# Kernel optimization log

Hardware: AMD Instinct MI355X
Metric: run time of the kernel (lower is better)

Reference implementation:

```python
import jax, jax.numpy as jnp
from jax import lax
import numpy as np

COMMITMENT_COST = 0.25
N_EMBED = 512
EDIM = 32


def _conv(x, w, b, stride, pad):
    # x: NCHW, w: OIHW (torch Conv2d layout)
    y = lax.conv_general_dilated(x, w, (stride, stride), [(pad, pad), (pad, pad)],
                                 dimension_numbers=("NCHW", "OIHW", "NCHW"))
    return y + b[None, :, None, None]


def _conv_t(x, w, b, stride, pad):
    # torch ConvTranspose2d weight layout: (in, out, kH, kW)
    k = w.shape[2]
    w_ = jnp.flip(w, (2, 3)).transpose(1, 0, 2, 3)  # -> OIHW
    p = k - 1 - pad
    y = lax.conv_general_dilated(x, w_, (1, 1), [(p, p), (p, p)],
                                 lhs_dilation=(stride, stride),
                                 dimension_numbers=("NCHW", "OIHW", "NCHW"))
    return y + b[None, :, None, None]


def setup_inputs() -> dict:
    key = jax.random.key(0)
    ks = jax.random.split(key, 9)
    rn = lambda k, s: jax.random.normal(k, s, jnp.float32) * 0.05
    return {
        "x": jax.random.normal(ks[0], (32, 3, 256, 256), jnp.float32),
        "e_w1": rn(ks[1], (64, 3, 4, 4)),    "e_b1": jnp.zeros((64,), jnp.float32),
        "e_w2": rn(ks[2], (128, 64, 4, 4)),  "e_b2": jnp.zeros((128,), jnp.float32),
        "e_w3": rn(ks[3], (32, 128, 3, 3)),  "e_b3": jnp.zeros((32,), jnp.float32),
        "embed": jax.random.uniform(ks[4], (N_EMBED, EDIM), jnp.float32,
                                    -1.0 / N_EMBED, 1.0 / N_EMBED),
        "d_w1": rn(ks[5], (32, 128, 3, 3)),  "d_b1": jnp.zeros((128,), jnp.float32),
        "d_w2": rn(ks[6], (128, 64, 4, 4)),  "d_b2": jnp.zeros((64,), jnp.float32),
        "d_w3": rn(ks[7], (64, 3, 4, 4)),    "d_b3": jnp.zeros((3,), jnp.float32),
    }


def reference(x, e_w1, e_b1, e_w2, e_b2, e_w3, e_b3, embed,
              d_w1, d_b1, d_w2, d_b2, d_w3, d_b3):
    # ---- encoder ----
    h = jax.nn.relu(_conv(x, e_w1, e_b1, 2, 1))   # [B,64,128,128]
    h = jax.nn.relu(_conv(h, e_w2, e_b2, 2, 1))   # [B,128,64,64]
    z = jax.nn.relu(_conv(h, e_w3, e_b3, 1, 1))   # [B,32,64,64]
    # ---- vector quantizer ----
    zp = z.transpose(0, 2, 3, 1)                  # BHWC
    zf = zp.reshape(-1, EDIM)                     # [N, 32]
    d = (zf ** 2).sum(1, keepdims=True) + (embed ** 2).sum(1) \
        - 2.0 * zf @ embed.T                      # [N, n_embed]
    idx = jnp.argmin(d, axis=1)                   # [N]
    z_q = embed[idx].reshape(zp.shape)            # gather == onehot @ embed
    sg = lax.stop_gradient
    loss = jnp.mean((sg(z_q) - zp) ** 2) + COMMITMENT_COST * jnp.mean((z_q - sg(zp)) ** 2)
    z_q_st = zp + sg(z_q - zp)                    # straight-through
    z_q_st = z_q_st.transpose(0, 3, 1, 2)         # back to NCHW
    # ---- decoder ----
    h = jax.nn.relu(_conv_t(z_q_st, d_w1, d_b1, 1, 1))  # [B,128,64,64]
    h = jax.nn.relu(_conv_t(h, d_w2, d_b2, 2, 1))       # [B,64,128,128]
    x_recon = _conv_t(h, d_w3, d_b3, 2, 1)              # [B,3,256,256]
    return x_recon, loss
```

## Files before the change

### kernel.cpp

```cpp
#include <hip/hip_runtime.h>


typedef __attribute__((ext_vector_type(8))) short     short8;
typedef __attribute__((ext_vector_type(4))) short     s16x4;
typedef __attribute__((ext_vector_type(8))) __bf16    bf16x8;
typedef __attribute__((ext_vector_type(4))) float     f32x4;
typedef __attribute__((ext_vector_type(4))) unsigned  uint32x4;

__device__ __forceinline__ float b2f(unsigned short b) {
  union { unsigned u; float f; } v; v.u = ((unsigned)b) << 16; return v.f;
}
__device__ __forceinline__ unsigned short f2b(float f) {
  union { float f; unsigned u; } v; v.f = f;
  unsigned r = v.u + 0x7FFF + ((v.u >> 16) & 1);
  return (unsigned short)(r >> 16);
}

__global__ __launch_bounds__(256) void prep1v_k(const float* __restrict__ w,
                                                unsigned short* __restrict__ wq) {
  const int i = blockIdx.x*256 + threadIdx.x;
  const int j = i & 7, l = (i >> 3) & 63, ni = (i >> 9) & 3, ks = i >> 11;
  const int k = ks*32 + (l >> 4)*8 + j;
  const int co = ni*16 + (l & 15);
  wq[i] = (k < 48) ? f2b(w[co*48 + k]) : (unsigned short)0;
}
__global__ __launch_bounds__(256) void prep2v_k(const float* __restrict__ w,
                                                unsigned short* __restrict__ wq) {
  const int i = blockIdx.x*256 + threadIdx.x;
  const int j = i & 7, l = (i >> 3) & 63, ni = (i >> 9) & 7, ks = i >> 12;
  const int lm = l & 15, lk = l >> 4;
  const int tap = ks >> 1, cc = ks & 1;
  const int co = ni*16 + lm, ci = cc*32 + lk*8 + j;
  wq[i] = f2b(w[(co*64 + ci)*16 + tap]);
}
__global__ __launch_bounds__(256) void prep3v_k(const float* __restrict__ w,
                                                unsigned short* __restrict__ wq) {
  const int i = blockIdx.x*256 + threadIdx.x;
  const int j = i & 7, l = (i >> 3) & 63, ni = (i >> 9) & 1, ks = i >> 10;
  const int lm = l & 15, lk = l >> 4;
  const int tap = ks >> 2, cf = ks & 3;
  const int co = ni*16 + lm, ci = cf*32 + lk*8 + j;
  wq[i] = f2b(w[(co*128 + ci)*9 + tap]);
}
__global__ __launch_bounds__(256) void prep4v_k(const float* __restrict__ w,
                                                unsigned short* __restrict__ wq) {
  const int i = blockIdx.x*256 + threadIdx.x;
  const int j = i & 7, l = (i >> 3) & 63, ni = (i >> 9) & 7, tap = i >> 12;
  const int lm = l & 15, lk = l >> 4;
  const int co = ni*16 + lm, ci = lk*8 + j;
  wq[i] = f2b(w[(ci*128 + co)*9 + (8 - tap)]);
}
__global__ __launch_bounds__(256) void prep5v_k(const float* __restrict__ w,
                                                unsigned short* __restrict__ wq) {
  const int i = blockIdx.x*256 + threadIdx.x;
  const int j = i & 7, l = (i >> 3) & 63, ni = (i >> 9) & 3;
  const int ks = (i >> 11) & 15, p = i >> 15;
  const int lm = l & 15, lk = l >> 4;
  const int py = p >> 1, px = p & 1;
  const int a = ks >> 3, b = (ks >> 2) & 1, cc = ks & 3;
  const int co = ni*16 + lm, ci = cc*32 + lk*8 + j;
  const int ky = 3 - 2*a - py, kx = 3 - 2*b - px;
  wq[i] = f2b(w[(ci*64 + co)*16 + ky*4 + kx]);
}
__global__ __launch_bounds__(256) void prep6_k(const float* __restrict__ w,
                                               unsigned short* __restrict__ wq) {
  const int i = blockIdx.x*256 + threadIdx.x;
  const int j = i & 7, l = (i >> 3) & 63, kc = (i >> 9) & 7, p = i >> 12;
  const int lm = l & 15, lk = l >> 4;
  const int a = kc >> 2, b = (kc >> 1) & 1, ch = kc & 1;
  const int ci = ch*32 + lk*8 + j, co = lm;
  const int py = p >> 1, px = p & 1;
  const int ky = 2 - 2*a + (1 - py), kx = 2 - 2*b + (1 - px);
  wq[i] = (co < 3) ? f2b(w[(ci*3 + co)*16 + ky*4 + kx]) : (unsigned short)0;
}
__global__ __launch_bounds__(256) void prepe_k(const float* __restrict__ emb,
    unsigned short* __restrict__ wqe, float* __restrict__ en) {
  const int i = blockIdx.x*256 + threadIdx.x;
  const int j = i & 7, l = (i >> 3) & 63, ni = (i >> 9) & 3, nc = i >> 11;
  const int lm = l & 15, lk = l >> 4;
  wqe[i] = f2b(emb[(nc*64 + ni*16 + lm)*32 + lk*8 + j]);
  if (i < 512) {
    float s = 0.f;
    #pragma unroll
    for (int k = 0; k < 32; ++k) {
      const float f = b2f(f2b(emb[i*32 + k]));
      s = fmaf(f, f, s);
    }
    en[i] = s;
  }
}

__global__ __launch_bounds__(256) void conv1m_k(const float* __restrict__ x,
    const unsigned short* __restrict__ wv, const float* __restrict__ bias,
    unsigned short* __restrict__ out) {
  __shared__ __align__(16) short RAW[12*264];
  __shared__ __align__(16) short IC[128*64];
  const int wid = ((blockIdx.x & 7) << 9) + (blockIdx.x >> 3);
  const int q = wid & 127, n = wid >> 7;
  for (int i = threadIdx.x; i < 396; i += 256)
    *(short8*)&RAW[i*8] = (short8)(short)0;
  __syncthreads();
  for (int s = threadIdx.x; s < 768; s += 256) {
    const int g = s >> 6, seg = s & 63;
    const int ci = g >> 2, ky = g & 3;
    const int iy = 2*q - 1 + ky;
    if (iy >= 0 && iy < 256) {
      const f32x4 v = *(const f32x4*)&x[((n*3 + ci)*256 + iy)*256 + seg*4];
      s16x4 sv;
      #pragma unroll
      for (int e = 0; e < 4; ++e) sv[e] = (short)f2b(v[e]);
      *(s16x4*)&RAW[g*264 + 4 + seg*4] = sv;
    }
  }
  __syncthreads();
  for (int s = threadIdx.x; s < 1024; s += 256) {
    const int kb = s & 7, ox = s >> 3;
    short8 v = (short8)(short)0;
    if (kb < 6) {
      const unsigned* u0 = (const unsigned*)&RAW[(2*kb  )*264 + 2*ox + 2];
      const unsigned* u1 = (const unsigned*)&RAW[(2*kb+1)*264 + 2*ox + 2];
      const unsigned a0 = u0[0], a1 = u0[1], a2 = u0[2];
      const unsigned b0 = u1[0], b1 = u1[1], b2 = u1[2];
      uint32x4 uv;
      uv[0] = (a0 >> 16) | (a1 << 16);
      uv[1] = (a1 >> 16) | (a2 << 16);
      uv[2] = (b0 >> 16) | (b1 << 16);
      uv[3] = (b1 >> 16) | (b2 << 16);
      v = __builtin_bit_cast(short8, uv);
    }
    const int bo = ((ox << 7) + (kb << 4)) ^ ((ox & 7) << 4);
    *(short8*)((char*)IC + bo) = v;
  }
  __syncthreads();
  const int w = threadIdx.x >> 6, l = threadIdx.x & 63;
  const int lm = l & 15, lk = l >> 4;
  f32x4 acc[2][4];
  #pragma unroll
  for (int mi = 0; mi < 2; ++mi)
    #pragma unroll
    for (int ni = 0; ni < 4; ++ni) acc[mi][ni] = (f32x4)0.0f;
  #pragma unroll
  for (int ks = 0; ks < 2; ++ks) {
    short8 bv[4];
    #pragma unroll
    for (int ni = 0; ni < 4; ++ni)
      bv[ni] = *(const short8*)(wv + (((ks*4 + ni)*64 + l) << 3));
    #pragma unroll
    for (int mi = 0; mi < 2; ++mi) {
      const int ox = w*32 + mi*16 + lm;
      const int bo = ((ox << 7) + (ks << 6) + (lk << 4)) ^ ((ox & 7) << 4);
      const short8 av = *(const short8*)((const char*)IC + bo);
      #pragma unroll
      for (int ni = 0; ni < 4; ++ni)
        acc[mi][ni] = __builtin_amdgcn_mfma_f32_16x16x32_bf16(
            __builtin_bit_cast(bf16x8, av),
            __builtin_bit_cast(bf16x8, bv[ni]),
            acc[mi][ni], 0, 0, 0);
    }
  }
  __syncthreads();
  #pragma unroll
  for (int mi = 0; mi < 2; ++mi)
    #pragma unroll
    for (int ni = 0; ni < 4; ++ni) {
      const int co = ni*16 + lm;
      const float bv = bias[co];
      #pragma unroll
      for (int r = 0; r < 4; ++r) {
        const int ox = w*32 + mi*16 + lk*4 + r;
        const int bo = ((ox << 7) + 2*co) ^ ((ox & 7) << 4);
        *(short*)((char*)IC + bo) = (short)f2b(fmaxf(acc[mi][ni][r] + bv, 0.f));
      }
    }
  __syncthreads();
  const long ob = ((long)(n*128 + q)) * 8192;
  for (int s = threadIdx.x; s < 1024; s += 256) {
    const int kb = s & 7, ox = s >> 3;
    const int bo = ((ox << 7) + (kb << 4)) ^ ((ox & 7) << 4);
    *(short8*)&out[ob + ox*64 + kb*8] = *(const short8*)((const char*)IC + bo);
  }
}

#define C2_LOAD(c) \
  _Pragma("unroll") \
  for (int s = 0; s < 9; ++s) { \
    st[s] = (short8)(short)0; \
    if (goff[s] >= 0) st[s] = *(const short8*)(in + goff[s] + (c)*32); \
  }
#define C2_WRITE \
  _Pragma("unroll") \
  for (int s = 0; s < 9; ++s) \
    if (lb[s] >= 0) *(short8*)((char*)IL + lb[s]) = st[s];
#define C2_COMPUTE(c) \
  _Pragma("unroll") \
  for (int t = 0; t < 16; ++t) { \
    const int ky = t >> 2, kx = t & 3; \
    const int p = 1 - (kx & 1), d = kx >> 1; \
    const short8 bv0 = *(const short8*)(wb + (t*2 + (c))*4096); \
    const short8 bv1 = *(const short8*)(wb + (t*2 + (c))*4096 + 512); \
    const char* Ab = (const char*)IL + (Bd0 + d*64); \
    const int imm0 = ((ky*2 + p)*66) << 6; \
    _Pragma("unroll") \
    for (int mi = 0; mi < 4; ++mi) { \
      const short8 av = *(const short8*)(Ab + imm0 + mi*1024); \
      acc[mi][0] = __builtin_amdgcn_mfma_f32_16x16x32_bf16( \
          __builtin_bit_cast(bf16x8, av), __builtin_bit_cast(bf16x8, bv0), \
          acc[mi][0], 0, 0, 0); \
      acc[mi][1] = __builtin_amdgcn_mfma_f32_16x16x32_bf16( \
          __builtin_bit_cast(bf16x8, av), __builtin_bit_cast(bf16x8, bv1), \
          acc[mi][1], 0, 0, 0); \
    } \
  }
__global__ __launch_bounds__(256) void conv2m_k(const unsigned short* __restrict__ in,
    const unsigned short* __restrict__ wv, const float* __restrict__ bias,
    unsigned short* __restrict__ out) {
  __shared__ short IL[8*66*32];
  const int wid = (blockIdx.x & 7)*256 + (blockIdx.x >> 3);
  const int q = wid & 63, n = wid >> 6;
  const int w = threadIdx.x >> 6, l = threadIdx.x & 63;
  const int lm = l & 15, lk = l >> 4;
  const int Bd0 = lm*64 + lk*16;
  const unsigned short* wb = wv + w*1024 + l*8;
  int goff[9], lb[9];
  #pragma unroll
  for (int s = 0; s < 9; ++s) {
    const int i = threadIdx.x + s*256;
    const int part = i & 3, e = i >> 2;
    const int idx = e % 66, rp = e / 66;
    const int r = rp >> 1, p = rp & 1;
    const int iy = 2*q - 1 + r, ix = 2*idx - p;
    const bool ok = (i < 2112) && iy >= 0 && iy < 128 && ix >= 0 && ix < 128;
    goff[s] = ok ? (((n*128 + iy)*128 + ix)*64 + part*8) : -1;
    lb[s]   = (i < 2112) ? (e*64 + part*16) : -1;
  }
  f32x4 acc[4][2];
  #pragma unroll
  for (int mi = 0; mi < 4; ++mi)
    #pragma unroll
    for (int ni = 0; ni < 2; ++ni) acc[mi][ni] = (f32x4)0.0f;
  short8 st[9];
  C2_LOAD(0); C2_WRITE;
  __syncthreads();
  C2_LOAD(1);
  C2_COMPUTE(0);
  __syncthreads();
  C2_WRITE;
  __syncthreads();
  C2_COMPUTE(1);
  #pragma unroll
  for (int mi = 0; mi < 4; ++mi)
    #pragma unroll
    for (int r = 0; r < 4; ++r) {
      const int ox = mi*16 + lk*4 + r;
      const int ob = ((n*64 + q)*64 + ox)*128;
      #pragma unroll
      for (int ni = 0; ni < 2; ++ni) {
        const int co = (w*2 + ni)*16 + lm;
        out[ob + co] = f2b(fmaxf(acc[mi][ni][r] + bias[co], 0.f));
      }
    }
}

#define C3_LOAD(c) \
  _Pragma("unroll") \
  for (int s = 0; s < 9; ++s) { \
    st[s] = (short8)(short)0; \
    if (goff[s] >= 0) st[s] = *(const short8*)(in + goff[s] + (c)*64); \
  }
#define C3_WRITE \
  _Pragma("unroll") \
  for (int s = 0; s < 9; ++s) \
    if (lb[s] >= 0) *(short8*)((char*)IL + lb[s]) = st[s];
#define C3_COMPUTE(c) \
  _Pragma("unroll") \
  for (int u = 0; u < 18; ++u) { \
    const int tap = u >> 1, cc = u & 1; \
    const int ky = tap / 3, kx = tap % 3; \
    const int ks = tap*4 + (c)*2 + cc; \
    const short8 bv0 = *(const short8*)(wb + ks*1024); \
    const short8 bv1 = *(const short8*)(wb + ks*1024 + 512); \
    const char* Ab = (const char*)IL + (Wc[kx][cc]); \
    const int imm0 = ky*8448; \
    _Pragma("unroll") \
    for (int mi = 0; mi < 2; ++mi) { \
      const short8 av = *(const short8*)(Ab + imm0 + mi*2048); \
      acc[mi][0] = __builtin_amdgcn_mfma_f32_16x16x32_bf16( \
          __builtin_bit_cast(bf16x8, av), __builtin_bit_cast(bf16x8, bv0), \
          acc[mi][0], 0, 0, 0); \
      acc[mi][1] = __builtin_amdgcn_mfma_f32_16x16x32_bf16( \
          __builtin_bit_cast(bf16x8, av), __builtin_bit_cast(bf16x8, bv1), \
          acc[mi][1], 0, 0, 0); \
    } \
  }
__global__ __launch_bounds__(256) void conv3v_k(const unsigned short* __restrict__ in,
    const unsigned short* __restrict__ wv, const float* __restrict__ bias,
    const unsigned short* __restrict__ wqe, const float* __restrict__ eng,
    const float* __restrict__ emb, float* __restrict__ zq,
    float* __restrict__ part) {
  __shared__ short IL[4*66*64];
  const int wid = (blockIdx.x & 7)*128 + (blockIdx.x >> 3);
  const int q = wid & 31, n = wid >> 5;
  const int w = threadIdx.x >> 6, l = threadIdx.x & 63;
  const int lm = l & 15, lk = l >> 4;
  const int row = w >> 1, oxb = (w & 1) * 32;
  int goff[9], lb[9];
  #pragma unroll
  for (int s = 0; s < 9; ++s) {
    const int i = threadIdx.x + s*256;
    const int part_ = i & 7, e = i >> 3;
    const int col = e % 66, r = e / 66;
    const int iy = 2*q - 1 + r, ix = col - 1;
    const bool ok = (i < 2112) && iy >= 0 && iy < 64 && ix >= 0 && ix < 64;
    goff[s] = ok ? (((n*64 + iy)*64 + ix)*128 + part_*8) : -1;
    lb[s]   = (i < 2112) ? ((e << 7) + ((part_ << 4) ^ ((col & 7) << 4))) : -1;
  }
  int Wc[3][2];
  #pragma unroll
  for (int kx = 0; kx < 3; ++kx) {
    const int e = oxb + lm + kx;
    Wc[kx][0] = row*8448 + (e << 7) + ((lk << 4) ^ ((e & 7) << 4));
    Wc[kx][1] = Wc[kx][0] ^ 0x40;
  }
  const unsigned short* wb = wv + l*8;
  f32x4 acc[2][2];
  #pragma unroll
  for (int mi = 0; mi < 2; ++mi)
    #pragma unroll
    for (int ni = 0; ni < 2; ++ni) acc[mi][ni] = (f32x4)0.0f;
  short8 st[9];
  C3_LOAD(0); C3_WRITE;
  __syncthreads();
  C3_LOAD(1);
  C3_COMPUTE(0);
  __syncthreads();
  C3_WRITE;
  __syncthreads();
  C3_COMPUTE(1);
  __syncthreads();
  short* ZB  = (short*)IL;
  float* ZF  = (float*)((char*)IL + 10240);
  int*  bidx = (int*)((char*)IL + 28672);
  float* red = (float*)((char*)IL + 29184);
  #pragma unroll
  for (int mi = 0; mi < 2; ++mi)
    #pragma unroll
    for (int ni = 0; ni < 2; ++ni) {
      const int co = ni*16 + lm;
      const float bv = bias[co];
      #pragma unroll
      for (int r = 0; r < 4; ++r) {
        const int pos = row*64 + oxb + mi*16 + lk*4 + r;
        const float v = fmaxf(acc[mi][ni][r] + bv, 0.f);
        ZB[pos*40 + co] = (short)f2b(v);
        ZF[pos*36 + co] = v;
      }
    }
  __syncthreads();
  short8 av[2];
  #pragma unroll
  for (int mi = 0; mi < 2; ++mi)
    av[mi] = *(const short8*)&ZB[(row*64 + oxb + mi*16 + lm)*40 + lk*8];
  float bd[2][4]; int bj[2][4];
  #pragma unroll
  for (int mi = 0; mi < 2; ++mi)
    #pragma unroll
    for (int r = 0; r < 4; ++r) { bd[mi][r] = 1e30f; bj[mi][r] = 0; }
  for (int nc = 0; nc < 8; ++nc) {
    f32x4 a2[2][4];
    #pragma unroll
    for (int mi = 0; mi < 2; ++mi)
      #pragma unroll
      for (int ni = 0; ni < 4; ++ni) a2[mi][ni] = (f32x4)0.0f;
    #pragma unroll
    for (int ni = 0; ni < 4; ++ni) {
      const short8 bv = *(const short8*)(wqe + (((nc*4 + ni)*64 + l) << 3));
      #pragma unroll
      for (int mi = 0; mi < 2; ++mi)
        a2[mi][ni] = __builtin_amdgcn_mfma_f32_16x16x32_bf16(
            __builtin_bit_cast(bf16x8, av[mi]),
            __builtin_bit_cast(bf16x8, bv),
            a2[mi][ni], 0, 0, 0);
    }
    #pragma unroll
    for (int ni = 0; ni < 4; ++ni) {
      const int j = nc*64 + ni*16 + lm;
      const float e_n = eng[j];
      #pragma unroll
      for (int mi = 0; mi < 2; ++mi)
        #pragma unroll
        for (int r = 0; r < 4; ++r) {
          const float d = fmaf(-2.f, a2[mi][ni][r], e_n);
          if (d < bd[mi][r]) { bd[mi][r] = d; bj[mi][r] = j; }
        }
    }
  }
  #pragma unroll
  for (int mi = 0; mi < 2; ++mi)
    #pragma unroll
    for (int r = 0; r < 4; ++r) {
      float d = bd[mi][r]; int j = bj[mi][r];
      #pragma unroll
      for (int off = 1; off < 16; off <<= 1) {
        const float od = __shfl_xor(d, off);
        const int   oj = __shfl_xor(j, off);
        if (od < d || (od == d && oj < j)) { d = od; j = oj; }
      }
      if (lm == 0) bidx[row*64 + oxb + mi*16 + lk*4 + r] = j;
    }
  __syncthreads();
  const int pl = threadIdx.x >> 1, hf = (threadIdx.x & 1) * 16;
  const int code = bidx[pl];
  const int oy2 = 2*q + (pl >> 6), ox2 = pl & 63;
  const long zqo = ((long)((n*64 + oy2)*64 + ox2)) * 32 + hf;
  float se = 0.f;
  #pragma unroll
  for (int qq = 0; qq < 4; ++qq) {
    const f32x4 ev = *(const f32x4*)&emb[code*32 + hf + qq*4];
    const f32x4 zv = *(const f32x4*)&ZF[pl*36 + hf + qq*4];
    *(f32x4*)&zq[zqo + qq*4] = ev;
    const f32x4 df = ev - zv;
    #pragma unroll
    for (int e = 0; e < 4; ++e) se = fmaf(df[e], df[e], se);
  }
  red[threadIdx.x] = se; __syncthreads();
  for (int s2 = 128; s2 > 0; s2 >>= 1) {
    if (threadIdx.x < s2) red[threadIdx.x] += red[threadIdx.x + s2];
    __syncthreads();
  }
  if (threadIdx.x == 0) part[blockIdx.x] = red[0];
}

__global__ __launch_bounds__(256) void d1m_k(const float* __restrict__ in,
    const unsigned short* __restrict__ wv, const float* __restrict__ bias,
    unsigned short* __restrict__ out) {
  __shared__ short IL[264*40];
  const int wid = (blockIdx.x & 7)*128 + (blockIdx.x >> 3);
  const int q = wid & 31, n = wid >> 5;
  const int w = threadIdx.x >> 6, l = threadIdx.x & 63;
  const int lm = l & 15, lk = l >> 4;
  const int row = w >> 1, oxb = (w & 1) * 32;
  for (int i = threadIdx.x; i < 1056; i += 256) {
    const int part = i & 3, e = i >> 2;
    const int col = e % 66, r = e / 66;
    const int iy = 2*q - 1 + r, ix = col - 1;
    short8 v = (short8)(short)0;
    if (iy >= 0 && iy < 64 && ix >= 0 && ix < 64) {
      const float* p = in + (((long)((n*64 + iy)*64 + ix)) * 32 + part*8);
      const f32x4 f0 = *(const f32x4*)p;
      const f32x4 f1 = *(const f32x4*)(p + 4);
      #pragma unroll
      for (int e2 = 0; e2 < 4; ++e2) {
        v[e2]     = (short)f2b(f0[e2]);
        v[e2 + 4] = (short)f2b(f1[e2]);
      }
    }
    *(short8*)&IL[e*40 + part*8] = v;
  }
  const unsigned short* wb = wv + l*8;
  int Wd[3];
  #pragma unroll
  for (int kx = 0; kx < 3; ++kx)
    Wd[kx] = row*5280 + (oxb + lm + kx)*80 + lk*16;
  __syncthreads();
  f32x4 acc[2][8];
  #pragma unroll
  for (int mi = 0; mi < 2; ++mi)
    #pragma unroll
    for (int ni = 0; ni < 8; ++ni) acc[mi][ni] = (f32x4)0.0f;
  #pragma unroll
  for (int tap = 0; tap < 9; ++tap) {
    const int ky = tap / 3, kx = tap % 3;
    short8 bv[8];
    #pragma unroll
    for (int ni = 0; ni < 8; ++ni)
      bv[ni] = *(const short8*)(wb + (tap*8 + ni)*512);
    const char* Ab = (const char*)IL + Wd[kx];
    const int imm0 = ky*5280;
    #pragma unroll
    for (int mi = 0; mi < 2; ++mi) {
      const short8 av = *(const short8*)(Ab + imm0 + mi*1280);
      #pragma unroll
      for (int ni = 0; ni < 8; ++ni)
        acc[mi][ni] = __builtin_amdgcn_mfma_f32_16x16x32_bf16(
            __builtin_bit_cast(bf16x8, av),
            __builtin_bit_cast(bf16x8, bv[ni]),
            acc[mi][ni], 0, 0, 0);
    }
  }
  const int oy = 2*q + row;
  #pragma unroll
  for (int mi = 0; mi < 2; ++mi)
    #pragma unroll
    for (int r = 0; r < 4; ++r) {
      const int ox = oxb + mi*16 + lk*4 + r;
      const int ob = ((n*64 + oy)*64 + ox)*128;
      #pragma unroll
      for (int ni = 0; ni < 8; ++ni) {
        const int co = ni*16 + lm;
        out[ob + co] = f2b(fmaxf(acc[mi][ni][r] + bias[co], 0.f));
      }
    }
}

#define CT2_LOAD(c) \
  _Pragma("unroll") \
  for (int s = 0; s < 7; ++s) { \
    st[s] = (short8)(short)0; \
    if (goff[s] >= 0) st[s] = *(const short8*)(in + goff[s] + (c)*64); \
  }
#define CT2_WRITE \
  _Pragma("unroll") \
  for (int s = 0; s < 7; ++s) \
    if (lb[s] >= 0) *(short8*)((char*)IL + lb[s]) = st[s];
#define CT2_COMPUTE(c) \
  _Pragma("unroll") \
  for (int u = 0; u < 8; ++u) { \
    const int a = u >> 2, b = (u >> 1) & 1, c1 = u & 1; \
    const int ks = (a << 3) | (b << 2) | (2*(c) + c1); \
    short8 bv[4]; \
    _Pragma("unroll") \
    for (int ni = 0; ni < 4; ++ni) \
      bv[ni] = *(const short8*)(wb + ks*2048 + ni*512); \
    const char* Ab = (const char*)IL + (pyb + Wb[b][c1]); \
    const int imm0 = a*8448; \
    _Pragma("unroll") \
    for (int mi = 0; mi < 4; ++mi) { \
      const short8 av = *(const short8*)(Ab + imm0 + mi*2048); \
      _Pragma("unroll") \
      for (int ni = 0; ni < 4; ++ni) \
        acc[mi][ni] = __builtin_amdgcn_mfma_f32_16x16x32_bf16( \
            __builtin_bit_cast(bf16x8, av), \
            __builtin_bit_cast(bf16x8, bv[ni]), \
            acc[mi][ni], 0, 0, 0); \
    } \
  }
__global__ __launch_bounds__(256) void convt2m_k(const unsigned short* __restrict__ in,
    const unsigned short* __restrict__ wv, const float* __restrict__ bias,
    unsigned short* __restrict__ out) {
  __shared__ short IL[3*66*64];
  const int wid = (blockIdx.x & 7)*256 + (blockIdx.x >> 3);
  const int q = wid & 63, n = wid >> 6;
  const int w = threadIdx.x >> 6, l = threadIdx.x & 63;
  const int py = w >> 1, px = w & 1;
  const int lm = l & 15, lk = l >> 4;
  int Wb[2][2];
  #pragma unroll
  for (int b = 0; b < 2; ++b) {
    const int e = lm + px + b;
    Wb[b][0] = (e << 7) + ((lk << 4) ^ ((e & 7) << 4));
    Wb[b][1] = Wb[b][0] ^ 0x40;
  }
  const int pyb = py * 8448;
  const unsigned short* wb = wv + w*32768 + l*8;
  int goff[7], lb[7];
  #pragma unroll
  for (int s = 0; s < 7; ++s) {
    const int i = threadIdx.x + s*256;
    const int part = i & 7, e = i >> 3;
    const int col = e % 66, r = e / 66;
    const int iy = q - 1 + r, ix = col - 1;
    const bool ok = (i < 1584) && iy >= 0 && iy < 64 && ix >= 0 && ix < 64;
    goff[s] = ok ? (((n*64 + iy)*64 + ix)*128 + part*8) : -1;
    lb[s]   = (i < 1584) ? ((e << 7) + ((part << 4) ^ ((col & 7) << 4))) : -1;
  }
  f32x4 acc[4][4];
  #pragma unroll
  for (int mi = 0; mi < 4; ++mi)
    #pragma unroll
    for (int ni = 0; ni < 4; ++ni) acc[mi][ni] = (f32x4)0.0f;
  short8 st[7];
  CT2_LOAD(0); CT2_WRITE;
  __syncthreads();
  CT2_LOAD(1);
  CT2_COMPUTE(0);
  __syncthreads();
  CT2_WRITE;
  __syncthreads();
  CT2_COMPUTE(1);
  const int oy = 2*q + py;
  #pragma unroll
  for (int mi = 0; mi < 4; ++mi)
    #pragma unroll
    for (int r = 0; r < 4; ++r) {
      const int ox = 2*(mi*16 + lk*4 + r) + px;
      const int ob = ((n*128 + oy)*128 + ox)*64;
      #pragma unroll
      for (int ni = 0; ni < 4; ++ni) {
        const int co = ni*16 + lm;
        out[ob + co] = f2b(fmaxf(acc[mi][ni][r] + bias[co], 0.f));
      }
    }
}

__global__ __launch_bounds__(256) void loss_k(const float* __restrict__ part,
                                              float* __restrict__ out) {
  __shared__ float red[256];
  const int t = threadIdx.x;
  float s = 0.f;
  #pragma unroll
  for (int q = 0; q < 4; ++q) s += part[t + q*256];
  red[t] = s; __syncthreads();
  for (int st = 128; st > 0; st >>= 1) {
    if (t < st) red[t] += red[t + st];
    __syncthreads();
  }
  if (t == 0) out[0] = red[0] * (1.25f / (131072.f * 32.f));
}

__global__ __launch_bounds__(256) void convt3m_k(const unsigned short* __restrict__ in,
    const unsigned short* __restrict__ wq6, const float* __restrict__ bias,
    float* __restrict__ out) {
  __shared__ short8 IL[3*8*66];
  const int h = blockIdx.x & 1, q = (blockIdx.x >> 1) & 127, n = blockIdx.x >> 8;
  for (int i = threadIdx.x; i < 1584; i += 256) {
    const int c8 = i & 7, t = i >> 3, ixl = t % 66, r = t / 66;
    const int iy = q - 1 + r, ix = h*64 - 1 + ixl;
    short8 v = (short8)(short)0;
    if (iy >= 0 && iy < 128 && ix >= 0 && ix < 128)
      v = *(const short8*)(in + (((long)(n*128 + iy)*128 + ix)*64 + c8*8));
    IL[(r*8 + c8)*66 + ixl] = v;
  }
  const int w = threadIdx.x >> 6, l = threadIdx.x & 63;
  const int py = w >> 1, px = w & 1;
  const int lm = l & 15, lk = l >> 4;
  short8 bfrag[8];
  #pragma unroll
  for (int kc = 0; kc < 8; ++kc)
    bfrag[kc] = *(const short8*)(wq6 + (((w*8 + kc)*64 + l) << 3));
  __syncthreads();
  f32x4 acc[4];
  #pragma unroll
  for (int mi = 0; mi < 4; ++mi) acc[mi] = (f32x4)0.0f;
  #pragma unroll
  for (int kc = 0; kc < 8; ++kc) {
    const int a = kc >> 2, b = (kc >> 1) & 1, ch = kc & 1;
    const int base = (((py + a)*8 + ch*4 + lk)*66) + px + b;
    #pragma unroll
    for (int mi = 0; mi < 4; ++mi) {
      const short8 av = *(const short8*)&IL[base + mi*16 + lm];
      acc[mi] = __builtin_amdgcn_mfma_f32_16x16x32_bf16(
          __builtin_bit_cast(bf16x8, av),
          __builtin_bit_cast(bf16x8, bfrag[kc]),
          acc[mi], 0, 0, 0);
    }
  }
  if (lm < 3) {
    const float bv = bias[lm];
    const int oy = 2*q + py;
    const long ob = ((long)(n*3 + lm))*65536 + oy*256;
    #pragma unroll
    for (int mi = 0; mi < 4; ++mi)
      #pragma unroll
      for (int r = 0; r < 4; ++r) {
        const int xq = mi*16 + lk*4 + r;
        out[ob + h*128 + 2*xq + px] = acc[mi][r] + bv;
      }
  }
}

extern "C" void kernel_launch(void* const* d_in, const int* in_sizes, int n_in,
                              void* d_out, int out_size, void* d_ws, size_t ws_size,
                              hipStream_t stream) {
  const float* x   = (const float*)d_in[0];
  const float* ew1 = (const float*)d_in[1];  const float* eb1 = (const float*)d_in[2];
  const float* ew2 = (const float*)d_in[3];  const float* eb2 = (const float*)d_in[4];
  const float* ew3 = (const float*)d_in[5];  const float* eb3 = (const float*)d_in[6];
  const float* emb = (const float*)d_in[7];
  const float* dw1 = (const float*)d_in[8];  const float* db1 = (const float*)d_in[9];
  const float* dw2 = (const float*)d_in[10]; const float* db2 = (const float*)d_in[11];
  const float* dw3 = (const float*)d_in[12]; const float* db3 = (const float*)d_in[13];
  float* out = (float*)d_out;

  uint8_t* w8 = (uint8_t*)d_ws;
  unsigned short* h1 = (unsigned short*)w8;
  unsigned short* h2 = (unsigned short*)(w8 + 67108864);
  uint8_t* zr = w8 + 100663296;
  float* zq  = (float*)(w8 + 117440512);
  unsigned short* wqe = (unsigned short*)zr;
  float* eng = (float*)(zr + 32768);
  float* part = (float*)(zr + 36864);
  unsigned short* wq3 = (unsigned short*)(zr + 40960);
  unsigned short* wq4 = (unsigned short*)(zr + 131072);
  unsigned short* wq5 = (unsigned short*)(zr + 262144);
  unsigned short* wq6 = (unsigned short*)(zr + 524288);
  unsigned short* wq2 = (unsigned short*)(w8 + 117440512);
  unsigned short* wq1 = (unsigned short*)(w8 + 117440512 + 335872);
  unsigned short* d1 = h2;
  unsigned short* d2 = h1;

  prepe_k<<<dim3(64),256,0,stream>>>(emb, wqe, eng);
  prep1v_k<<<dim3(16),256,0,stream>>>(ew1, wq1);
  prep2v_k<<<dim3(512),256,0,stream>>>(ew2, wq2);
  prep3v_k<<<dim3(144),256,0,stream>>>(ew3, wq3);
  prep4v_k<<<dim3(144),256,0,stream>>>(dw1, wq4);
  prep5v_k<<<dim3(512),256,0,stream>>>(dw2, wq5);
  prep6_k<<<dim3(64),256,0,stream>>>(dw3, wq6);
  conv1m_k<<<dim3(4096),256,0,stream>>>(x, wq1, eb1, h1);
  conv2m_k<<<dim3(2048),256,0,stream>>>(h1, wq2, eb2, h2);
  conv3v_k<<<dim3(1024),256,0,stream>>>(h2, wq3, eb3, wqe, eng, emb, zq, part);
  loss_k<<<dim3(1),256,0,stream>>>(part, out + 6291456);
  d1m_k<<<dim3(1024),256,0,stream>>>(zq, wq4, db1, d1);
  convt2m_k<<<dim3(2048),256,0,stream>>>(d1, wq5, db2, d2);
  convt3m_k<<<dim3(8192),256,0,stream>>>(d2, wq6, db3, out);
}
```

Before: 355.8 us.

## Stage conv epilogues through LDS for coalesced stores; merge weight prep kernels

Four conv kernels (conv2, decoder conv1, convt2, convt3) now write their bias+ReLU results into shared memory first. They then emit contiguous 16-byte vector stores (or coalesced row stores for the final fp32 output) instead of scattered 2-byte per-lane global writes. The seven weight-preparation kernels are merged into one launch with block-range dispatch to cut launch overhead. The staging adds extra barriers and reuses the input LDS buffer, which must be large enough for the padded tiles.

```diff
diff --git a/kernel.cpp b/kernel.cpp
--- a/kernel.cpp
+++ b/kernel.cpp
@@ -16,77 +16,75 @@
   return (unsigned short)(r >> 16);
 }
 
-__global__ __launch_bounds__(256) void prep1v_k(const float* __restrict__ w,
-                                                unsigned short* __restrict__ wq) {
-  const int i = blockIdx.x*256 + threadIdx.x;
-  const int j = i & 7, l = (i >> 3) & 63, ni = (i >> 9) & 3, ks = i >> 11;
-  const int k = ks*32 + (l >> 4)*8 + j;
-  const int co = ni*16 + (l & 15);
-  wq[i] = (k < 48) ? f2b(w[co*48 + k]) : (unsigned short)0;
-}
-__global__ __launch_bounds__(256) void prep2v_k(const float* __restrict__ w,
-                                                unsigned short* __restrict__ wq) {
-  const int i = blockIdx.x*256 + threadIdx.x;
-  const int j = i & 7, l = (i >> 3) & 63, ni = (i >> 9) & 7, ks = i >> 12;
-  const int lm = l & 15, lk = l >> 4;
-  const int tap = ks >> 1, cc = ks & 1;
-  const int co = ni*16 + lm, ci = cc*32 + lk*8 + j;
-  wq[i] = f2b(w[(co*64 + ci)*16 + tap]);
-}
-__global__ __launch_bounds__(256) void prep3v_k(const float* __restrict__ w,
-                                                unsigned short* __restrict__ wq) {
-  const int i = blockIdx.x*256 + threadIdx.x;
-  const int j = i & 7, l = (i >> 3) & 63, ni = (i >> 9) & 1, ks = i >> 10;
-  const int lm = l & 15, lk = l >> 4;
-  const int tap = ks >> 2, cf = ks & 3;
-  const int co = ni*16 + lm, ci = cf*32 + lk*8 + j;
-  wq[i] = f2b(w[(co*128 + ci)*9 + tap]);
-}
-__global__ __launch_bounds__(256) void prep4v_k(const float* __restrict__ w,
-                                                unsigned short* __restrict__ wq) {
-  const int i = blockIdx.x*256 + threadIdx.x;
-  const int j = i & 7, l = (i >> 3) & 63, ni = (i >> 9) & 7, tap = i >> 12;
-  const int lm = l & 15, lk = l >> 4;
-  const int co = ni*16 + lm, ci = lk*8 + j;
-  wq[i] = f2b(w[(ci*128 + co)*9 + (8 - tap)]);
-}
-__global__ __launch_bounds__(256) void prep5v_k(const float* __restrict__ w,
-                                                unsigned short* __restrict__ wq) {
-  const int i = blockIdx.x*256 + threadIdx.x;
-  const int j = i & 7, l = (i >> 3) & 63, ni = (i >> 9) & 3;
-  const int ks = (i >> 11) & 15, p = i >> 15;
-  const int lm = l & 15, lk = l >> 4;
-  const int py = p >> 1, px = p & 1;
-  const int a = ks >> 3, b = (ks >> 2) & 1, cc = ks & 3;
-  const int co = ni*16 + lm, ci = cc*32 + lk*8 + j;
-  const int ky = 3 - 2*a - py, kx = 3 - 2*b - px;
-  wq[i] = f2b(w[(ci*64 + co)*16 + ky*4 + kx]);
-}
-__global__ __launch_bounds__(256) void prep6_k(const float* __restrict__ w,
-                                               unsigned short* __restrict__ wq) {
-  const int i = blockIdx.x*256 + threadIdx.x;
-  const int j = i & 7, l = (i >> 3) & 63, kc = (i >> 9) & 7, p = i >> 12;
-  const int lm = l & 15, lk = l >> 4;
-  const int a = kc >> 2, b = (kc >> 1) & 1, ch = kc & 1;
-  const int ci = ch*32 + lk*8 + j, co = lm;
-  const int py = p >> 1, px = p & 1;
-  const int ky = 2 - 2*a + (1 - py), kx = 2 - 2*b + (1 - px);
-  wq[i] = (co < 3) ? f2b(w[(ci*3 + co)*16 + ky*4 + kx]) : (unsigned short)0;
-}
-__global__ __launch_bounds__(256) void prepe_k(const float* __restrict__ emb,
-    unsigned short* __restrict__ wqe, float* __restrict__ en) {
-  const int i = blockIdx.x*256 + threadIdx.x;
-  const int j = i & 7, l = (i >> 3) & 63, ni = (i >> 9) & 3, nc = i >> 11;
-  const int lm = l & 15, lk = l >> 4;
-  wqe[i] = f2b(emb[(nc*64 + ni*16 + lm)*32 + lk*8 + j]);
-  if (i < 512) {
-    float s = 0.f;
-    #pragma unroll
-    for (int k = 0; k < 32; ++k) {
-      const float f = b2f(f2b(emb[i*32 + k]));
-      s = fmaf(f, f, s);
-    }
-    en[i] = s;
+__global__ __launch_bounds__(256) void prepall_k(
+    const float* __restrict__ ew1, const float* __restrict__ ew2,
+    const float* __restrict__ ew3, const float* __restrict__ dw1,
+    const float* __restrict__ dw2, const float* __restrict__ dw3,
+    const float* __restrict__ emb,
+    unsigned short* __restrict__ wq1, unsigned short* __restrict__ wq2,
+    unsigned short* __restrict__ wq3, unsigned short* __restrict__ wq4,
+    unsigned short* __restrict__ wq5, unsigned short* __restrict__ wq6,
+    unsigned short* __restrict__ wqe, float* __restrict__ eng) {
+  const int b = blockIdx.x;
+  if (b < 64) {
+    const int i = b*256 + threadIdx.x;
+    const int j = i & 7, l = (i >> 3) & 63, ni = (i >> 9) & 3, nc = i >> 11;
+    const int lm = l & 15, lk = l >> 4;
+    wqe[i] = f2b(emb[(nc*64 + ni*16 + lm)*32 + lk*8 + j]);
+    if (i < 512) {
+      float s = 0.f;
+      #pragma unroll
+      for (int k = 0; k < 32; ++k) {
+        const float f = b2f(f2b(emb[i*32 + k]));
+        s = fmaf(f, f, s);
+      }
+      eng[i] = s;
+    }
+  } else if (b < 80) {
+    const int i = (b - 64)*256 + threadIdx.x;
+    const int j = i & 7, l = (i >> 3) & 63, ni = (i >> 9) & 3, ks = i >> 11;
+    const int k = ks*32 + (l >> 4)*8 + j;
+    const int co = ni*16 + (l & 15);
+    wq1[i] = (k < 48) ? f2b(ew1[co*48 + k]) : (unsigned short)0;
+  } else if (b < 592) {
+    const int i = (b - 80)*256 + threadIdx.x;
+    const int j = i & 7, l = (i >> 3) & 63, ni = (i >> 9) & 7, ks = i >> 12;
+    const int lm = l & 15, lk = l >> 4;
+    const int tap = ks >> 1, cc = ks & 1;
+    const int co = ni*16 + lm, ci = cc*32 + lk*8 + j;
+    wq2[i] = f2b(ew2[(co*64 + ci)*16 + tap]);
+  } else if (b < 736) {
+    const int i = (b - 592)*256 + threadIdx.x;
+    const int j = i & 7, l = (i >> 3) & 63, ni = (i >> 9) & 1, ks = i >> 10;
+    const int lm = l & 15, lk = l >> 4;
+    const int tap = ks >> 2, cf = ks & 3;
+    const int co = ni*16 + lm, ci = cf*32 + lk*8 + j;
+    wq3[i] = f2b(ew3[(co*128 + ci)*9 + tap]);
+  } else if (b < 880) {
+    const int i = (b - 736)*256 + threadIdx.x;
+    const int j = i & 7, l = (i >> 3) & 63, ni = (i >> 9) & 7, tap = i >> 12;
+    const int lm = l & 15, lk = l >> 4;
+    const int co = ni*16 + lm, ci = lk*8 + j;
+    wq4[i] = f2b(dw1[(ci*128 + co)*9 + (8 - tap)]);
+  } else if (b < 1392) {
+    const int i = (b - 880)*256 + threadIdx.x;
+    const int j = i & 7, l = (i >> 3) & 63, ni = (i >> 9) & 3;
+    const int ks = (i >> 11) & 15, p = i >> 15;
+    const int lm = l & 15, lk = l >> 4;
+    const int py = p >> 1, px = p & 1;
+    const int a = ks >> 3, bb = (ks >> 2) & 1, cc = ks & 3;
+    const int co = ni*16 + lm, ci = cc*32 + lk*8 + j;
+    const int ky = 3 - 2*a - py, kx = 3 - 2*bb - px;
+    wq5[i] = f2b(dw2[(ci*64 + co)*16 + ky*4 + kx]);
+  } else {
+    const int i = (b - 1392)*256 + threadIdx.x;
+    const int j = i & 7, l = (i >> 3) & 63, kc = (i >> 9) & 7, p = i >> 12;
+    const int lm = l & 15, lk = l >> 4;
+    const int a = kc >> 2, bb = (kc >> 1) & 1, ch = kc & 1;
+    const int ci = ch*32 + lk*8 + j, co = lm;
+    const int py = p >> 1, px = p & 1;
+    const int ky = 2 - 2*a + (1 - py), kx = 2 - 2*bb + (1 - px);
+    wq6[i] = (co < 3) ? f2b(dw3[(ci*3 + co)*16 + ky*4 + kx]) : (unsigned short)0;
   }
 }
 
@@ -247,18 +245,27 @@
   C2_WRITE;
   __syncthreads();
   C2_COMPUTE(1);
+  __syncthreads();
+  short* PB = (short*)IL;
   #pragma unroll
   for (int mi = 0; mi < 4; ++mi)
     #pragma unroll
     for (int r = 0; r < 4; ++r) {
       const int ox = mi*16 + lk*4 + r;
-      const int ob = ((n*64 + q)*64 + ox)*128;
       #pragma unroll
       for (int ni = 0; ni < 2; ++ni) {
         const int co = (w*2 + ni)*16 + lm;
-        out[ob + co] = f2b(fmaxf(acc[mi][ni][r] + bias[co], 0.f));
+        PB[ox*144 + co] = (short)f2b(fmaxf(acc[mi][ni][r] + bias[co], 0.f));
       }
     }
+  __syncthreads();
+  {
+    const int pos = threadIdx.x >> 2, coq = (threadIdx.x & 3) << 5;
+    const long ob = ((long)((n*64 + q)*64 + pos))*128 + coq;
+    #pragma unroll
+    for (int u2 = 0; u2 < 4; ++u2)
+      *(short8*)&out[ob + u2*8] = *(const short8*)&PB[pos*144 + coq + u2*8];
+  }
 }
 
 #define C3_LOAD(c) \
@@ -487,19 +494,30 @@
             acc[mi][ni], 0, 0, 0);
     }
   }
-  const int oy = 2*q + row;
-  #pragma unroll
-  for (int mi = 0; mi < 2; ++mi)
-    #pragma unroll
-    for (int r = 0; r < 4; ++r) {
-      const int ox = oxb + mi*16 + lk*4 + r;
-      const int ob = ((n*64 + oy)*64 + ox)*128;
-      #pragma unroll
-      for (int ni = 0; ni < 8; ++ni) {
-        const int co = ni*16 + lm;
-        out[ob + co] = f2b(fmaxf(acc[mi][ni][r] + bias[co], 0.f));
-      }
-    }
+  short* PB = (short*)IL;
+  #pragma unroll
+  for (int rp = 0; rp < 2; ++rp) {
+    __syncthreads();
+    if (row == rp) {
+      #pragma unroll
+      for (int mi = 0; mi < 2; ++mi)
+        #pragma unroll
+        for (int r = 0; r < 4; ++r) {
+          const int ox = oxb + mi*16 + lk*4 + r;
+          #pragma unroll
+          for (int ni = 0; ni < 8; ++ni) {
+            const int co = ni*16 + lm;
+            PB[ox*144 + co] = (short)f2b(fmaxf(acc[mi][ni][r] + bias[co], 0.f));
+          }
+        }
+    }
+    __syncthreads();
+    const int pos = threadIdx.x >> 2, coq = (threadIdx.x & 3) << 5;
+    const long ob = ((long)((n*64 + 2*q + rp)*64 + pos))*128 + coq;
+    #pragma unroll
+    for (int u2 = 0; u2 < 4; ++u2)
+      *(short8*)&out[ob + u2*8] = *(const short8*)&PB[pos*144 + coq + u2*8];
+  }
 }
 
 #define CT2_LOAD(c) \
@@ -577,19 +595,31 @@
   CT2_WRITE;
   __syncthreads();
   CT2_COMPUTE(1);
-  const int oy = 2*q + py;
-  #pragma unroll
-  for (int mi = 0; mi < 4; ++mi)
-    #pragma unroll
-    for (int r = 0; r < 4; ++r) {
-      const int ox = 2*(mi*16 + lk*4 + r) + px;
-      const int ob = ((n*128 + oy)*128 + ox)*64;
-      #pragma unroll
-      for (int ni = 0; ni < 4; ++ni) {
-        const int co = ni*16 + lm;
-        out[ob + co] = f2b(fmaxf(acc[mi][ni][r] + bias[co], 0.f));
+  short* PB = (short*)IL;
+  #pragma unroll
+  for (int half = 0; half < 2; ++half) {
+    __syncthreads();
+    #pragma unroll
+    for (int mi = 0; mi < 4; ++mi)
+      #pragma unroll
+      for (int r = 0; r < 4; ++r) {
+        const int ox = 2*(mi*16 + lk*4 + r) + px;
+        const int pos = py*128 + ox;
+        #pragma unroll
+        for (int nn = 0; nn < 2; ++nn) {
+          const int co = (half*2 + nn)*16 + lm;
+          PB[pos*40 + (co & 31)] =
+              (short)f2b(fmaxf(acc[mi][half*2 + nn][r] + bias[co], 0.f));
+        }
       }
-    }
+    __syncthreads();
+    const int pos = threadIdx.x;
+    const long ob = ((long)((n*128 + 2*q + (pos >> 7))*128 + (pos & 127)))*64
+                    + half*32;
+    #pragma unroll
+    for (int u2 = 0; u2 < 4; ++u2)
+      *(short8*)&out[ob + u2*8] = *(const short8*)&PB[pos*40 + u2*8];
+  }
 }
 
 __global__ __launch_bounds__(256) void loss_k(const float* __restrict__ part,
@@ -644,17 +674,22 @@
           acc[mi], 0, 0, 0);
     }
   }
+  __syncthreads();
+  float* PB3 = (float*)IL;
   if (lm < 3) {
     const float bv = bias[lm];
-    const int oy = 2*q + py;
-    const long ob = ((long)(n*3 + lm))*65536 + oy*256;
     #pragma unroll
     for (int mi = 0; mi < 4; ++mi)
       #pragma unroll
       for (int r = 0; r < 4; ++r) {
         const int xq = mi*16 + lk*4 + r;
-        out[ob + h*128 + 2*xq + px] = acc[mi][r] + bv;
+        PB3[(lm*2 + py)*128 + 2*xq + px] = acc[mi][r] + bv;
       }
+  }
+  __syncthreads();
+  for (int t = threadIdx.x; t < 768; t += 256) {
+    const int co = t >> 8, rem = t & 255, pyl = rem >> 7, xx = rem & 127;
+    out[((long)(n*3 + co))*65536 + (2*q + pyl)*256 + h*128 + xx] = PB3[t];
   }
 }
 
@@ -688,13 +723,8 @@
   unsigned short* d1 = h2;
   unsigned short* d2 = h1;
 
-  prepe_k<<<dim3(64),256,0,stream>>>(emb, wqe, eng);
-  prep1v_k<<<dim3(16),256,0,stream>>>(ew1, wq1);
-  prep2v_k<<<dim3(512),256,0,stream>>>(ew2, wq2);
-  prep3v_k<<<dim3(144),256,0,stream>>>(ew3, wq3);
-  prep4v_k<<<dim3(144),256,0,stream>>>(dw1, wq4);
-  prep5v_k<<<dim3(512),256,0,stream>>>(dw2, wq5);
-  prep6_k<<<dim3(64),256,0,stream>>>(dw3, wq6);
+  prepall_k<<<dim3(1456),256,0,stream>>>(ew1, ew2, ew3, dw1, dw2, dw3, emb,
+                                         wq1, wq2, wq3, wq4, wq5, wq6, wqe, eng);
   conv1m_k<<<dim3(4096),256,0,stream>>>(x, wq1, eb1, h1);
   conv2m_k<<<dim3(2048),256,0,stream>>>(h1, wq2, eb2, h2);
   conv3v_k<<<dim3(1024),256,0,stream>>>(h2, wq3, eb3, wqe, eng, emb, zq, part);
```

After: 340.5 us. -4.3%, faster.
